# Optimization experiments

Measured on AMD Instinct MI355X. Metric: run time of the kernel, lower is better.

Reference implementation:

```python
import jax, jax.numpy as jnp
import numpy as np

QMAX = 127.0  # torch.iinfo(torch.int8).max


def setup_inputs() -> dict:
    key = jax.random.key(0)
    k1, k2 = jax.random.split(key)
    input_act = jax.random.normal(k1, (4, 2048, 4096), dtype=jnp.float32)
    # nn.Linear weight: [out_features, in_features], fp weights pre-quantization
    weight = jax.random.normal(k2, (4096, 4096), dtype=jnp.float32) * 0.02
    return {"input_act": input_act, "weight": weight}


def reference(input_act, weight):
    # --- weight_quant (per-channel over in_features) ---
    w_scale = jnp.max(jnp.abs(weight), axis=-1, keepdims=True) / QMAX      # [O, 1]
    w_q = jnp.round(weight / w_scale).astype(jnp.int8)                      # int8 weight

    # --- activation quant (per-token over last dim) ---
    a_scale = jnp.max(jnp.abs(input_act), axis=-1, keepdims=True) / QMAX    # [B, S, 1]
    x_q = jnp.round(input_act / a_scale).astype(jnp.int8)                   # int8 acts

    # --- int8 GEMM with int32 accumulation (torch._int_mm semantics) ---
    # [B, S, K] @ [K, O] -> [B, S, O]
    acc = jnp.matmul(x_q.astype(jnp.int32), w_q.T.astype(jnp.int32))        # exact int32

    # --- dequant: scale = input_act_scale * weight_scale.T, then cast to fp16 ---
    scale = a_scale * w_scale.T[None, :, :]                                 # [B, S, O]
    out = (acc.astype(jnp.float32) * scale).astype(jnp.float16)
    return out
```

## Files before the change

kernel.cpp:

```cpp
#include <hip/hip_runtime.h>
#include <hip/hip_fp16.h>
#include <cstdint>

typedef int v4i __attribute__((ext_vector_type(4)));

#define AS1C(p) ((const __attribute__((address_space(1))) void*)(p))
#define AS3(p)  ((__attribute__((address_space(3))) void*)(p))

__global__ __launch_bounds__(256) void quant_rows(const float* __restrict__ X,
                                                  int8_t* __restrict__ Q,
                                                  float* __restrict__ scales,
                                                  int K) {
    const int row = blockIdx.x;
    const float4* xv = (const float4*)(X + (size_t)row * K);
    const int nv = K >> 2;

    float m = 0.0f;
    for (int i = threadIdx.x; i < nv; i += 256) {
        float4 v = xv[i];
        m = fmaxf(m, fabsf(v.x));
        m = fmaxf(m, fabsf(v.y));
        m = fmaxf(m, fabsf(v.z));
        m = fmaxf(m, fabsf(v.w));
    }
    for (int off = 32; off > 0; off >>= 1)
        m = fmaxf(m, __shfl_xor(m, off, 64));

    __shared__ float wmax[4];
    __shared__ float s_sc;
    const int lane = threadIdx.x & 63;
    const int wv = threadIdx.x >> 6;
    if (lane == 0) wmax[wv] = m;
    __syncthreads();
    if (threadIdx.x == 0) {
        float mm = fmaxf(fmaxf(wmax[0], wmax[1]), fmaxf(wmax[2], wmax[3]));
        float sc = mm / 127.0f;
        scales[row] = sc;
        s_sc = sc;
    }
    __syncthreads();
    const float sc = s_sc;

    char4* qv = (char4*)(Q + (size_t)row * K);
    for (int i = threadIdx.x; i < nv; i += 256) {
        float4 v = xv[i];
        char4 q;
        q.x = (signed char)(int)rintf(v.x / sc);
        q.y = (signed char)(int)rintf(v.y / sc);
        q.z = (signed char)(int)rintf(v.z / sc);
        q.w = (signed char)(int)rintf(v.w / sc);
        qv[i] = q;
    }
}

__global__ __launch_bounds__(512, 2) void gemm_i8(const int8_t* __restrict__ Aq,
                                                  const int8_t* __restrict__ Bq,
                                                  const float* __restrict__ a_scale,
                                                  const float* __restrict__ w_scale,
                                                  float* __restrict__ out) {
    extern __shared__ __align__(16) int8_t smem[];

    const int K = 4096;
    const int bid = blockIdx.x;
    const int wg  = (bid & 7) * 64 + (bid >> 3);
    const int n0 = (wg & 15) * 256;
    const int m0 = (wg >> 4) * 256;

    const int tid  = threadIdx.x;
    const int lane = tid & 63;
    const int wid  = tid >> 6;
    const int wm   = wid >> 2;
    const int wn   = wid & 3;

    const int rsel  = lane & 15;
    const int kswz  = ((lane >> 4) << 4) ^ (((rsel >> 1) & 3) << 4);
    const int abase = (wm * 128 + rsel) * 64 + kswz;
    const int bbase = 16384 + (wn * 64 + rsel) * 64 + kswz;

    const int strow = tid >> 2;
    const int stswz = ((strow >> 1) & 3) << 4;
    const int stcol = ((tid & 3) << 4) ^ stswz;
    const int8_t* gA = Aq + (size_t)(m0 + strow) * K + stcol;
    const int8_t* gB = Bq + (size_t)(n0 + strow) * K + stcol;
    const size_t rstep = (size_t)128 * K;
    const int ldsst = wid * 1024;

    v4i acc[8][4] = {};
    v4i aFa[8], aFb[8], bFa[4], bFb[4];

#define STAGE(buf, kt) do {                                                          \
    int8_t* _d = smem + (buf) * 32768;                                               \
    const int8_t* _a = gA + (size_t)(kt) * 64;                                       \
    const int8_t* _b = gB + (size_t)(kt) * 64;                                       \
    __builtin_amdgcn_global_load_lds(AS1C(_a),         AS3(_d + ldsst),         16, 0, 0); \
    __builtin_amdgcn_global_load_lds(AS1C(_a + rstep), AS3(_d + 8192  + ldsst), 16, 0, 0); \
    __builtin_amdgcn_global_load_lds(AS1C(_b),         AS3(_d + 16384 + ldsst), 16, 0, 0); \
    __builtin_amdgcn_global_load_lds(AS1C(_b + rstep), AS3(_d + 24576 + ldsst), 16, 0, 0); \
  } while (0)

#define KSTEP(u, CA, CB, NA, NB, kt4) do {                                           \
    const int kt  = (kt4) + (u);                                                     \
    const int8_t* bufN = smem + (((u) + 1) & 3) * 32768;                             \
    const int ktp = (kt + 3 < 64) ? (kt + 3) : 63;                                   \
    asm volatile("s_waitcnt vmcnt(4)" ::: "memory");                                 \
    __builtin_amdgcn_s_barrier();                                                    \
    _Pragma("unroll")                                                                \
    for (int mt = 0; mt < 8; ++mt)                                                   \
        NA[mt] = *(const v4i*)(bufN + abase + mt * 1024);                            \
    STAGE(((u) + 3) & 3, ktp);                                                       \
    __builtin_amdgcn_sched_barrier(0);                                               \
    __builtin_amdgcn_s_setprio(1);                                                   \
    _Pragma("unroll")                                                                \
    for (int nt = 0; nt < 4; ++nt) {                                                 \
        _Pragma("unroll")                                                            \
        for (int mt = 0; mt < 8; ++mt)                                               \
            acc[mt][nt] = __builtin_amdgcn_mfma_i32_16x16x64_i8(                     \
                CA[mt], CB[nt], acc[mt][nt], 0, 0, 0);                               \
        NB[nt] = *(const v4i*)(bufN + bbase + nt * 1024);                            \
    }                                                                                \
    __builtin_amdgcn_s_setprio(0);                                                   \
  } while (0)

    STAGE(0, 0); STAGE(1, 1); STAGE(2, 2);
    asm volatile("s_waitcnt vmcnt(8)" ::: "memory");
    __builtin_amdgcn_s_barrier();
#pragma unroll
    for (int mt = 0; mt < 8; ++mt) aFa[mt] = *(const v4i*)(smem + abase + mt * 1024);
#pragma unroll
    for (int nt = 0; nt < 4; ++nt) bFa[nt] = *(const v4i*)(smem + bbase + nt * 1024);

    for (int kt4 = 0; kt4 < 64; kt4 += 4) {
        KSTEP(0, aFa, bFa, aFb, bFb, kt4);
        KSTEP(1, aFb, bFb, aFa, bFa, kt4);
        KSTEP(2, aFa, bFa, aFb, bFb, kt4);
        KSTEP(3, aFb, bFb, aFa, bFa, kt4);
    }

    const int r0  = (lane >> 4) << 2;
    const int col = lane & 15;
#pragma unroll
    for (int mt = 0; mt < 8; ++mt) {
        const int tbase = m0 + wm * 128 + mt * 16 + r0;
        float as[4];
#pragma unroll
        for (int r = 0; r < 4; ++r) as[r] = a_scale[tbase + r];
#pragma unroll
        for (int nt = 0; nt < 4; ++nt) {
            const int o = n0 + wn * 64 + nt * 16 + col;
            const float wsc = w_scale[o];
#pragma unroll
            for (int r = 0; r < 4; ++r) {
                float v = (float)acc[mt][nt][r] * as[r] * wsc;
                out[(size_t)(tbase + r) * 4096 + o] = __half2float(__float2half_rn(v));
            }
        }
    }
#undef KSTEP
#undef STAGE
}

extern "C" void kernel_launch(void* const* d_in, const int* in_sizes, int n_in,
                              void* d_out, int out_size, void* d_ws, size_t ws_size,
                              hipStream_t stream) {
    const float* input_act = (const float*)d_in[0];
    const float* weight    = (const float*)d_in[1];
    float* out = (float*)d_out;

    const int K = 4096, O = 4096, T = 8192;

    int8_t* x_q = (int8_t*)d_ws;
    int8_t* w_q = x_q + (size_t)T * K;
    float* a_scale = (float*)(w_q + (size_t)O * K);
    float* w_scale = a_scale + T;

    static bool attr_done = false;
    if (!attr_done) {
        hipFuncSetAttribute(reinterpret_cast<const void*>(gemm_i8),
                            hipFuncAttributeMaxDynamicSharedMemorySize, 131072);
        attr_done = true;
    }

    quant_rows<<<T, 256, 0, stream>>>(input_act, x_q, a_scale, K);
    quant_rows<<<O, 256, 0, stream>>>(weight, w_q, w_scale, K);

    dim3 grid(512);
    gemm_i8<<<grid, 512, 131072, stream>>>(x_q, w_q, a_scale, w_scale, out);
}
```

Before: 195.7 us.

## Interleave LDS fragment loads and global-to-LDS stages with MFMA groups

The GEMM main loop is restructured so each k-step runs four groups, and each group issues its LDS fragment reads and one global_load_lds before its MFMAs. Previously all A fragments and the whole stage were issued up front. The aim is to spread memory traffic across the MFMA stream so issue slots and LDS bandwidth overlap better with the matrix units, with sched_barriers fixing the order. The quant kernel also preloads four float4s per thread into registers, so it reads the input once instead of twice. This relies on K being exactly 4096 with 256 threads.

```diff
diff --git a/kernel.cpp b/kernel.cpp
--- a/kernel.cpp
+++ b/kernel.cpp
@@ -13,15 +13,16 @@
                                                   int K) {
     const int row = blockIdx.x;
     const float4* xv = (const float4*)(X + (size_t)row * K);
-    const int nv = K >> 2;
+
+    float4 v[4];
+#pragma unroll
+    for (int j = 0; j < 4; ++j) v[j] = xv[threadIdx.x + (j << 8)];
 
     float m = 0.0f;
-    for (int i = threadIdx.x; i < nv; i += 256) {
-        float4 v = xv[i];
-        m = fmaxf(m, fabsf(v.x));
-        m = fmaxf(m, fabsf(v.y));
-        m = fmaxf(m, fabsf(v.z));
-        m = fmaxf(m, fabsf(v.w));
+#pragma unroll
+    for (int j = 0; j < 4; ++j) {
+        m = fmaxf(m, fmaxf(fmaxf(fabsf(v[j].x), fabsf(v[j].y)),
+                           fmaxf(fabsf(v[j].z), fabsf(v[j].w))));
     }
     for (int off = 32; off > 0; off >>= 1)
         m = fmaxf(m, __shfl_xor(m, off, 64));
@@ -42,14 +43,14 @@
     const float sc = s_sc;
 
     char4* qv = (char4*)(Q + (size_t)row * K);
-    for (int i = threadIdx.x; i < nv; i += 256) {
-        float4 v = xv[i];
+#pragma unroll
+    for (int j = 0; j < 4; ++j) {
         char4 q;
-        q.x = (signed char)(int)rintf(v.x / sc);
-        q.y = (signed char)(int)rintf(v.y / sc);
-        q.z = (signed char)(int)rintf(v.z / sc);
-        q.w = (signed char)(int)rintf(v.w / sc);
-        qv[i] = q;
+        q.x = (signed char)(int)rintf(v[j].x / sc);
+        q.y = (signed char)(int)rintf(v[j].y / sc);
+        q.z = (signed char)(int)rintf(v[j].z / sc);
+        q.w = (signed char)(int)rintf(v[j].w / sc);
+        qv[threadIdx.x + (j << 8)] = q;
     }
 }
 
@@ -98,26 +99,37 @@
     __builtin_amdgcn_global_load_lds(AS1C(_b + rstep), AS3(_d + 24576 + ldsst), 16, 0, 0); \
   } while (0)
 
+#define GROUP(g, CA, CB, NA, NB, gsrc, goff)  do {                                   \
+    NA[2*(g)]     = *(const v4i*)(bufN + abase + (2*(g))     * 1024);                \
+    NA[2*(g) + 1] = *(const v4i*)(bufN + abase + (2*(g) + 1) * 1024);                \
+    NB[(g)]       = *(const v4i*)(bufN + bbase + (g) * 1024);                        \
+    __builtin_amdgcn_global_load_lds(AS1C(gsrc), AS3(pD + (goff) + ldsst), 16, 0, 0);\
+    _Pragma("unroll")                                                                \
+    for (int nt = 0; nt < 4; ++nt) {                                                 \
+        acc[2*(g)][nt] = __builtin_amdgcn_mfma_i32_16x16x64_i8(                      \
+            CA[2*(g)], CB[nt], acc[2*(g)][nt], 0, 0, 0);                             \
+        acc[2*(g)+1][nt] = __builtin_amdgcn_mfma_i32_16x16x64_i8(                    \
+            CA[2*(g)+1], CB[nt], acc[2*(g)+1][nt], 0, 0, 0);                         \
+    }                                                                                \
+  } while (0)
+
 #define KSTEP(u, CA, CB, NA, NB, kt4) do {                                           \
     const int kt  = (kt4) + (u);                                                     \
     const int8_t* bufN = smem + (((u) + 1) & 3) * 32768;                             \
+    int8_t* pD = smem + (((u) + 3) & 3) * 32768;                                     \
     const int ktp = (kt + 3 < 64) ? (kt + 3) : 63;                                   \
+    const int8_t* _a = gA + (size_t)ktp * 64;                                        \
+    const int8_t* _b = gB + (size_t)ktp * 64;                                        \
     asm volatile("s_waitcnt vmcnt(4)" ::: "memory");                                 \
     __builtin_amdgcn_s_barrier();                                                    \
-    _Pragma("unroll")                                                                \
-    for (int mt = 0; mt < 8; ++mt)                                                   \
-        NA[mt] = *(const v4i*)(bufN + abase + mt * 1024);                            \
-    STAGE(((u) + 3) & 3, ktp);                                                       \
+    __builtin_amdgcn_s_setprio(1);                                                   \
+    GROUP(0, CA, CB, NA, NB, _a,         0);                                         \
     __builtin_amdgcn_sched_barrier(0);                                               \
-    __builtin_amdgcn_s_setprio(1);                                                   \
-    _Pragma("unroll")                                                                \
-    for (int nt = 0; nt < 4; ++nt) {                                                 \
-        _Pragma("unroll")                                                            \
-        for (int mt = 0; mt < 8; ++mt)                                               \
-            acc[mt][nt] = __builtin_amdgcn_mfma_i32_16x16x64_i8(                     \
-                CA[mt], CB[nt], acc[mt][nt], 0, 0, 0);                               \
-        NB[nt] = *(const v4i*)(bufN + bbase + nt * 1024);                            \
-    }                                                                                \
+    GROUP(1, CA, CB, NA, NB, _a + rstep, 8192);                                      \
+    __builtin_amdgcn_sched_barrier(0);                                               \
+    GROUP(2, CA, CB, NA, NB, _b,         16384);                                     \
+    __builtin_amdgcn_sched_barrier(0);                                               \
+    GROUP(3, CA, CB, NA, NB, _b + rstep, 24576);                                     \
     __builtin_amdgcn_s_setprio(0);                                                   \
   } while (0)
 
@@ -156,6 +168,7 @@
         }
     }
 #undef KSTEP
+#undef GROUP
 #undef STAGE
 }
 
```

Measured after the change: 180.8 us. -7.6%, faster.
